# Kernel tuning notes

Measured on AMD Instinct MI355X. Metric: run time of the kernel, lower is better.

The kernel has to match this reference:

```python
import jax, jax.numpy as jnp
import numpy as np

BATCH = 4
N1 = 131072   # stage-1 voxels (total over batch)
N2 = 32768    # stage-2 (stride-2 downsampled) voxels
D_MODEL = 128
D_INNER = 2 * D_MODEL
D_STATE = 16
D_CONV = 4
DT_RANK = 8   # ceil(d_model / 16)
EPS = 1e-5


def _ln(x, g, b):
    mu = x.mean(-1, keepdims=True)
    v = ((x - mu) ** 2).mean(-1, keepdims=True)
    return (x - mu) * jax.lax.rsqrt(v + EPS) * g + b


def _causal_conv(x, w, b):
    # x: [B,L,Di], w: [Di,K] -> depthwise causal conv1d
    y = jax.lax.conv_general_dilated(
        x.transpose(0, 2, 1), w[:, None, :], (1,), [(D_CONV - 1, 0)],
        dimension_numbers=('NCH', 'OIH', 'NCH'), feature_group_count=D_INNER)
    return y.transpose(0, 2, 1) + b


def _mamba_block(x, ln_g, ln_b, in_w, conv_w, conv_b, xproj_w, dtproj_w, dtproj_b, A_log, Dp, out_w):
    # create_block: LayerNorm -> Mamba mixer (selective scan); returns hidden states
    h = _ln(x, ln_g, ln_b)
    xz = h @ in_w.T                          # [B,L,2*Di]
    xc, z = jnp.split(xz, 2, axis=-1)
    xc = jax.nn.silu(_causal_conv(xc, conv_w, conv_b))
    dbl = xc @ xproj_w.T                     # [B,L,dt_rank+2*d_state]
    dt = jax.nn.softplus(dbl[..., :DT_RANK] @ dtproj_w.T + dtproj_b)  # [B,L,Di]
    Bm = dbl[..., DT_RANK:DT_RANK + D_STATE]
    Cm = dbl[..., DT_RANK + D_STATE:]
    A = -jnp.exp(A_log)                      # [Di,ds]

    def step(hst, inp):
        dt_t, b_t, c_t, u_t = inp            # [B,Di],[B,ds],[B,ds],[B,Di]
        hst = jnp.exp(dt_t[..., None] * A) * hst + (dt_t * u_t)[..., None] * b_t[:, None, :]
        return hst, jnp.einsum('bds,bs->bd', hst, c_t)

    h0 = jnp.zeros((x.shape[0], D_INNER, D_STATE), x.dtype)
    xs = (dt.transpose(1, 0, 2), Bm.transpose(1, 0, 2), Cm.transpose(1, 0, 2), xc.transpose(1, 0, 2))
    _, ys = jax.lax.scan(step, h0, xs)       # ys: [L,B,Di]
    y = ys.transpose(1, 0, 2) + xc * Dp
    y = y * jax.nn.silu(z)
    return y @ out_w.T


def _mamba_params(key):
    ks = jax.random.split(key, 6)
    s = lambda k, sh, sc: jax.random.normal(k, sh, jnp.float32) * sc
    return dict(
        ln_g=jnp.ones((D_MODEL,), jnp.float32), ln_b=jnp.zeros((D_MODEL,), jnp.float32),
        in_w=s(ks[0], (2 * D_INNER, D_MODEL), 0.05),
        conv_w=s(ks[1], (D_INNER, D_CONV), 0.2), conv_b=jnp.zeros((D_INNER,), jnp.float32),
        xproj_w=s(ks[2], (DT_RANK + 2 * D_STATE, D_INNER), 0.05),
        dtproj_w=s(ks[3], (D_INNER, DT_RANK), 0.1), dtproj_b=s(ks[4], (D_INNER,), 0.1),
        A_log=jnp.log(jnp.tile(jnp.arange(1, D_STATE + 1, dtype=jnp.float32), (D_INNER, 1))),
        D=jnp.ones((D_INNER,), jnp.float32),
        out_w=s(ks[5], (D_MODEL, D_INNER), 0.05))


def setup_inputs():
    key = jax.random.key(0)
    k = jax.random.split(key, 10)
    inp = {
        'feats_s1': jax.random.normal(k[0], (N1, D_MODEL), jnp.float32),
        'feats_s2': jax.random.normal(k[1], (N2, D_MODEL), jnp.float32),
        'pos_s1': jax.random.uniform(k[2], (N1, 3), jnp.float32),
        'pos_s2': jax.random.uniform(k[3], (N2, 3), jnp.float32),
        'hilbert_s1': jax.random.randint(k[4], (N1,), 0, 1 << 30, jnp.int32),
        'hilbert_s2': jax.random.randint(k[5], (N2,), 0, 1 << 30, jnp.int32),
        'pe_w': jax.random.normal(k[6], (D_MODEL, 3), jnp.float32) * 0.1,
        'pe_b': jnp.zeros((D_MODEL,), jnp.float32),
        'norm_g': jnp.ones((D_MODEL,), jnp.float32), 'norm_b': jnp.zeros((D_MODEL,), jnp.float32),
        'normb_g': jnp.ones((D_MODEL,), jnp.float32), 'normb_b': jnp.zeros((D_MODEL,), jnp.float32),
    }
    for pref, kk in (('m1_', k[7]), ('m2_', k[8])):
        for n, v in _mamba_params(kk).items():
            inp[pref + n] = v
    return inp


def _forward(feats_s1, feats_s2, pos_s1, pos_s2, pe_w, pe_b, norm_g, norm_b, normb_g, normb_b,
             m1_ln_g, m1_ln_b, m1_in_w, m1_conv_w, m1_conv_b, m1_xproj_w, m1_dtproj_w, m1_dtproj_b, m1_A_log, m1_D, m1_out_w,
             m2_ln_g, m2_ln_b, m2_in_w, m2_conv_w, m2_conv_b, m2_xproj_w, m2_dtproj_w, m2_dtproj_b, m2_A_log, m2_D, m2_out_w,
             hilbert_s1, hilbert_s2):
    L1, L2 = N1 // BATCH, N2 // BATCH
    m1 = (m1_ln_g, m1_ln_b, m1_in_w, m1_conv_w, m1_conv_b, m1_xproj_w, m1_dtproj_w, m1_dtproj_b, m1_A_log, m1_D, m1_out_w)
    m2 = (m2_ln_g, m2_ln_b, m2_in_w, m2_conv_w, m2_conv_b, m2_xproj_w, m2_dtproj_w, m2_dtproj_b, m2_A_log, m2_D, m2_out_w)

    # stage 2: hilbert-order forward scan through mamba_layer1
    f2 = (feats_s2 + pos_s2 @ pe_w.T + pe_b).reshape(BATCH, L2, D_MODEL)
    o2 = jnp.argsort(hilbert_s2.reshape(BATCH, L2), axis=-1)          # inds_curt_to_next
    seq2 = jnp.take_along_axis(f2, o2[..., None], axis=1)
    out2 = _mamba_block(seq2, *m1)
    back2 = jnp.take_along_axis(out2, jnp.argsort(o2, axis=-1)[..., None], axis=1).reshape(N2, D_MODEL)
    out_s2 = _ln(back2, norm_g, norm_b)

    # stage 1: flipped hilbert-order (backward) scan through mamba_layer2
    f1 = (feats_s1 + pos_s1 @ pe_w.T + pe_b).reshape(BATCH, L1, D_MODEL)
    o1 = jnp.argsort(hilbert_s1.reshape(BATCH, L1), axis=-1)
    seq1 = jnp.take_along_axis(f1, o1[..., None], axis=1)[:, ::-1, :]
    out1 = _mamba_block(seq1, *m2)[:, ::-1, :]
    back1 = jnp.take_along_axis(out1, jnp.argsort(o1, axis=-1)[..., None], axis=1).reshape(N1, D_MODEL)
    out_s1 = _ln(back1, normb_g, normb_b)

    return jnp.concatenate([out_s1, out_s2], axis=0)   # [N1+N2, d_model]


def reference(feats_s1, feats_s2, pos_s1, pos_s2, pe_w, pe_b, norm_g, norm_b, normb_g, normb_b,
              m1_ln_g, m1_ln_b, m1_in_w, m1_conv_w, m1_conv_b, m1_xproj_w, m1_dtproj_w, m1_dtproj_b, m1_A_log, m1_D, m1_out_w,
              m2_ln_g, m2_ln_b, m2_in_w, m2_conv_w, m2_conv_b, m2_xproj_w, m2_dtproj_w, m2_dtproj_b, m2_A_log, m2_D, m2_out_w,
              hilbert_s1, hilbert_s2):
    return _forward(feats_s1, feats_s2, pos_s1, pos_s2, pe_w, pe_b, norm_g, norm_b, normb_g, normb_b,
                    m1_ln_g, m1_ln_b, m1_in_w, m1_conv_w, m1_conv_b, m1_xproj_w, m1_dtproj_w, m1_dtproj_b, m1_A_log, m1_D, m1_out_w,
                    m2_ln_g, m2_ln_b, m2_in_w, m2_conv_w, m2_conv_b, m2_xproj_w, m2_dtproj_w, m2_dtproj_b, m2_A_log, m2_D, m2_out_w,
                    hilbert_s1, hilbert_s2)
```

## Files before the change

kernel.cpp:

```cpp
#include <hip/hip_runtime.h>
#include <hip/hip_bf16.h>

#define DEV __device__ __forceinline__

constexpr int BATCH_ = 4;
constexpr int N1_ = 131072;
constexpr int N2_ = 32768;
constexpr int L1_ = N1_ / BATCH_;
constexpr int L2_ = N2_ / BATCH_;
constexpr int DM_ = 128;
constexpr int DI_ = 256;
constexpr int DS_ = 16;
constexpr int DTR_ = 8;
constexpr int TOT_ = N1_ + N2_;

constexpr int TA_ = 32;
constexpr int TAH_ = TA_ + 3;
constexpr int NTILE1_ = L1_ / TA_;
constexpr int NTILE2_ = L2_ / TA_;
constexpr int NTILES_ = 4 * NTILE1_ + 4 * NTILE2_;

constexpr int TS_ = 128;
constexpr int NCH1_ = L1_ / TS_;
constexpr int NCH2_ = L2_ / TS_;
constexpr int NCHUNKS_ = 4 * NCH1_ + 4 * NCH2_;

constexpr int NST_ = 160;

constexpr int PADR_ = 16;
constexpr int SR1_ = L1_ + 2 * PADR_;
constexpr int SR2_ = L2_ + 2 * PADR_;
constexpr int RTOT_ = 4 * SR1_ + 4 * SR2_;

constexpr int IN1_OFF = 0;
constexpr int IN2_OFF = 65536;
constexpr int XP1_OFF = 131072;
constexpr int XP2_OFF = 143360;
constexpr int OW1_OFF = 155648;
constexpr int OW2_OFF = 188416;
constexpr int W16_TOT = 221184;

typedef short short8 __attribute__((ext_vector_type(8)));
typedef float f32x4 __attribute__((ext_vector_type(4)));

struct MP {
  const float* ln_g; const float* ln_b; const float* in_w;
  const float* conv_w; const float* conv_b; const float* xproj_w;
  const float* dtproj_w; const float* dtproj_b; const float* A_log;
  const float* Dp; const float* out_w;
};

DEV float softplusf(float x) {
  return fmaxf(x, 0.f) + __logf(1.f + __expf(-fabsf(x)));
}

DEV unsigned short f2bf(float f) {
  unsigned u = __builtin_bit_cast(unsigned, f);
  u += 0x7fffu + ((u >> 16) & 1u);
  return (unsigned short)(u >> 16);
}
DEV float bf2f(unsigned short s) {
  unsigned u = ((unsigned)s) << 16;
  return __builtin_bit_cast(float, u);
}

DEV void sort_tile_info(int tile, int& seg, int& tis, int& slotbase) {
  if (tile < 128) { seg = tile >> 5; tis = tile & 31; slotbase = seg * L1_; }
  else { seg = 4 + ((tile - 128) >> 3); tis = (tile - 128) & 7; slotbase = N1_ + (seg - 4) * L2_; }
}

__global__ __launch_bounds__(256) void k_prep(
    const float* __restrict__ in_w1, const float* __restrict__ xp1,
    const float* __restrict__ ow1,
    const float* __restrict__ in_w2, const float* __restrict__ xp2,
    const float* __restrict__ ow2,
    unsigned short* __restrict__ w16)
{
  const int i = blockIdx.x * 256 + threadIdx.x;
  if (i >= W16_TOT) return;
  float v;
  if (i < IN2_OFF) v = in_w1[i - IN1_OFF];
  else if (i < XP1_OFF) v = in_w2[i - IN2_OFF];
  else if (i < XP2_OFF) {
    const int j = i - XP1_OFF; const int r = j >> 8;
    v = (r < 40) ? xp1[j] : 0.f;
  } else if (i < OW1_OFF) {
    const int j = i - XP2_OFF; const int r = j >> 8;
    v = (r < 40) ? xp2[j] : 0.f;
  } else if (i < OW2_OFF) v = ow1[i - OW1_OFF];
  else v = ow2[i - OW2_OFF];
  w16[i] = f2bf(v);
}

__global__ __launch_bounds__(256) void k_hist(
    const int* __restrict__ hil1, const int* __restrict__ hil2,
    const unsigned* __restrict__ ksrc, unsigned* __restrict__ histg,
    int shift, int pass0)
{
  const int tile = blockIdx.x;
  int seg, tis, slotbase;
  sort_tile_info(tile, seg, tis, slotbase);
  const int tid = threadIdx.x;
  __shared__ unsigned h[1024];
  #pragma unroll
  for (int i = 0; i < 4; ++i) h[i * 256 + tid] = 0;
  __syncthreads();
  #pragma unroll
  for (int it = 0; it < 4; ++it) {
    const int li = tis * 1024 + it * 256 + tid;
    unsigned k;
    if (pass0) k = (unsigned)(seg < 4 ? hil1[seg * L1_ + li] : hil2[(seg - 4) * L2_ + li]);
    else       k = ksrc[slotbase + li];
    atomicAdd(&h[(k >> shift) & 1023u], 1u);
  }
  __syncthreads();
  #pragma unroll
  for (int i = 0; i < 4; ++i)
    histg[tile * 1024 + i * 256 + tid] = h[i * 256 + tid];
}

__global__ __launch_bounds__(256) void k_scanoff(
    const unsigned* __restrict__ histg, unsigned* __restrict__ offg)
{
  const int seg = blockIdx.x;
  const int ntiles = seg < 4 ? 32 : 8;
  const int tilebase = seg < 4 ? seg * 32 : 128 + (seg - 4) * 8;
  const int tid = threadIdx.x;
  const int d0 = tid * 4;
  unsigned tot[4] = {0, 0, 0, 0};
  for (int t = 0; t < ntiles; ++t) {
    const unsigned* hp = &histg[(size_t)(tilebase + t) * 1024 + d0];
    tot[0] += hp[0]; tot[1] += hp[1]; tot[2] += hp[2]; tot[3] += hp[3];
  }
  unsigned lp[4]; unsigned s = 0;
  #pragma unroll
  for (int j = 0; j < 4; ++j) { lp[j] = s; s += tot[j]; }
  const int lane = tid & 63, wv = tid >> 6;
  unsigned inc = s;
  #pragma unroll
  for (int off = 1; off < 64; off <<= 1) {
    unsigned v = (unsigned)__shfl_up((int)inc, off, 64);
    if (lane >= off) inc += v;
  }
  __shared__ unsigned wsum[4];
  if (lane == 63) wsum[wv] = inc;
  __syncthreads();
  unsigned wbase = 0;
  for (int w = 0; w < 4; ++w) if (w < wv) wbase += wsum[w];
  const unsigned base = wbase + inc - s;
  #pragma unroll
  for (int j = 0; j < 4; ++j) {
    unsigned run = base + lp[j];
    for (int t = 0; t < ntiles; ++t) {
      offg[(size_t)(tilebase + t) * 1024 + d0 + j] = run;
      run += histg[(size_t)(tilebase + t) * 1024 + d0 + j];
    }
  }
}

__global__ __launch_bounds__(256) void k_scatter(
    const int* __restrict__ hil1, const int* __restrict__ hil2,
    const unsigned* __restrict__ ksrc, const int* __restrict__ isrc,
    const unsigned* __restrict__ offg,
    unsigned* __restrict__ kdst, int* __restrict__ idst,
    int* __restrict__ o_all, int shift, int pass0, int last)
{
  const int tile = blockIdx.x;
  int seg, tis, slotbase;
  sort_tile_info(tile, seg, tis, slotbase);
  const int tid = threadIdx.x;
  const int lane = tid & 63, wv = tid >> 6;
  __shared__ unsigned runb[1024];
  __shared__ unsigned wcnt[4 * 1024];
  #pragma unroll
  for (int i = 0; i < 4; ++i) runb[i * 256 + tid] = offg[(size_t)tile * 1024 + i * 256 + tid];
  #pragma unroll
  for (int it = 0; it < 4; ++it) {
    #pragma unroll
    for (int i = 0; i < 16; ++i) wcnt[i * 256 + tid] = 0;
    __syncthreads();
    const int li = tis * 1024 + it * 256 + tid;
    unsigned k; int v;
    if (pass0) {
      k = (unsigned)(seg < 4 ? hil1[seg * L1_ + li] : hil2[(seg - 4) * L2_ + li]);
      v = li;
    } else {
      k = ksrc[slotbase + li]; v = isrc[slotbase + li];
    }
    const unsigned d = (k >> shift) & 1023u;
    unsigned long long m = ~0ull;
    #pragma unroll
    for (int b = 0; b < 10; ++b) {
      const unsigned long long bb = __ballot((int)((d >> b) & 1u));
      m &= ((d >> b) & 1u) ? bb : ~bb;
    }
    const unsigned lrank = (unsigned)__popcll(m & ((1ull << lane) - 1ull));
    wcnt[wv * 1024 + d] = (unsigned)__popcll(m);
    __syncthreads();
    unsigned prior = runb[d];
    for (int w = 0; w < 3; ++w) if (w < wv) prior += wcnt[w * 1024 + d];
    const unsigned pos = prior + lrank;
    if (last) o_all[slotbase + pos] = v;
    else { kdst[slotbase + pos] = k; idst[slotbase + pos] = v; }
    __syncthreads();
    #pragma unroll
    for (int i = 0; i < 4; ++i) {
      const int dd = i * 256 + tid;
      runb[dd] += wcnt[dd] + wcnt[1024 + dd] + wcnt[2048 + dd] + wcnt[3072 + dd];
    }
    __syncthreads();
  }
}

__global__ __launch_bounds__(256) void k_gather(
    const float* __restrict__ feats1, const float* __restrict__ feats2,
    const float* __restrict__ pos1, const float* __restrict__ pos2,
    const float* __restrict__ pe_w, const float* __restrict__ pe_b,
    MP p1, MP p2, const int* __restrict__ o_all,
    unsigned* __restrict__ seq_g)
{
  const int wv = threadIdx.x >> 6, lane = threadIdx.x & 63;
  const int prow = blockIdx.x * 4 + wv;
  if (prow >= RTOT_) return;
  int seg, within;
  if (prow < 4 * SR1_) { seg = prow / SR1_; within = prow - seg * SR1_; }
  else { const int r = prow - 4 * SR1_; seg = 4 + r / SR2_; within = r - (seg - 4) * SR2_; }
  const bool is1 = seg < 4;
  const int b = is1 ? seg : seg - 4;
  const int L = is1 ? L1_ : L2_;
  const int p = within - PADR_;
  unsigned outw = 0;
  if (p >= 0 && p < L) {
    const int slotbase = is1 ? b * L1_ : N1_ + b * L2_;
    const int orig = o_all[slotbase + p];
    const MP P = is1 ? p2 : p1;
    const float* fr = (is1 ? feats1 + (size_t)b * L1_ * DM_
                           : feats2 + (size_t)b * L2_ * DM_) + (size_t)orig * DM_;
    const float* pr = (is1 ? pos1 + (size_t)b * L1_ * 3
                           : pos2 + (size_t)b * L2_ * 3) + (size_t)orig * 3;
    const int c0 = 2 * lane;
    const float2 f = *(const float2*)(fr + c0);
    const float q0 = pr[0], q1 = pr[1], q2 = pr[2];
    float x0 = f.x + q0 * pe_w[c0 * 3 + 0] + q1 * pe_w[c0 * 3 + 1] + q2 * pe_w[c0 * 3 + 2] + pe_b[c0];
    float x1 = f.y + q0 * pe_w[c0 * 3 + 3] + q1 * pe_w[c0 * 3 + 4] + q2 * pe_w[c0 * 3 + 5] + pe_b[c0 + 1];
    float s = x0 + x1, qq = x0 * x0 + x1 * x1;
    #pragma unroll
    for (int off = 32; off; off >>= 1) {
      s += __shfl_xor(s, off, 64);
      qq += __shfl_xor(qq, off, 64);
    }
    const float mu = s * (1.f / 128.f);
    const float rs = rsqrtf(qq * (1.f / 128.f) - mu * mu + 1e-5f);
    const unsigned short o0 = f2bf((x0 - mu) * rs * P.ln_g[c0]     + P.ln_b[c0]);
    const unsigned short o1 = f2bf((x1 - mu) * rs * P.ln_g[c0 + 1] + P.ln_b[c0 + 1]);
    outw = (unsigned)o0 | ((unsigned)o1 << 16);
  }
  seq_g[(size_t)prow * 64 + lane] = outw;
}

constexpr int HB_ = 136;
constexpr int XB_ = 264;
constexpr int OFF_HB16 = TAH_ * XB_ * 2;
constexpr int SMEM_A = OFF_HB16 + 48 * HB_ * 2;

__global__ __launch_bounds__(256) void k_phaseA(
    MP p1, MP p2,
    const unsigned short* __restrict__ seq_g,
    const unsigned short* __restrict__ w16,
    __hip_bfloat16* __restrict__ xc_g, __hip_bfloat16* __restrict__ z_g,
    float* __restrict__ dbl_g)
{
  const int blk = blockIdx.x;
  bool is1; int b, tile;
  if (blk < 4 * NTILE1_) { is1 = true; b = blk / NTILE1_; tile = blk % NTILE1_; }
  else { const int r = blk - 4 * NTILE1_; is1 = false; b = r / NTILE2_; tile = r % NTILE2_; }
  const int slotbase = is1 ? b * L1_ : N1_ + b * L2_;
  const MP P = is1 ? p2 : p1;
  const unsigned short* iw16 = w16 + (is1 ? IN2_OFF : IN1_OFF);
  const unsigned short* xp16 = w16 + (is1 ? XP2_OFF : XP1_OFF);
  const int segrow0 = is1 ? b * SR1_ : 4 * SR1_ + b * SR2_;
  const unsigned short* seq = seq_g + (size_t)segrow0 * DM_;
  const bool rev = is1;
  const int t0 = tile * TA_;
  const int pstart = rev ? t0 : t0 - 3;
  const int lsh = rev ? 0 : 3;

  __shared__ char smem[SMEM_A];
  unsigned short* xcb16 = (unsigned short*)smem;
  unsigned short* hb16 = (unsigned short*)(smem + OFF_HB16);
  unsigned short* xc16 = xcb16;

  const int tid = threadIdx.x;
  const int lane = tid & 63, wv = tid >> 6;
  const int l15 = lane & 15, quad = lane >> 4;

  {
    unsigned* hz = (unsigned*)hb16;
    for (int i = tid; i < 13 * (HB_ / 2); i += 256)
      hz[TAH_ * (HB_ / 2) + i] = 0;
    const unsigned short* src = seq + (size_t)(PADR_ + pstart) * DM_;
    #pragma unroll
    for (int i = tid; i < TAH_ * 16; i += 256) {
      const int r = i >> 4, c = (i & 15) * 8;
      *(uint4*)(hb16 + r * HB_ + c) = *(const uint4*)(src + (size_t)r * DM_ + c);
    }
  }
  __syncthreads();
  {
    short8 afr[3][4];
    #pragma unroll
    for (int mt = 0; mt < 3; ++mt)
      #pragma unroll
      for (int t = 0; t < 4; ++t)
        afr[mt][t] = *(const short8*)(hb16 + (mt * 16 + l15) * HB_ + t * 32 + quad * 8);
    for (int nn = 0; nn < 8; ++nn) {
      const int ntile = nn * 4 + wv;
      f32x4 acc[3];
      #pragma unroll
      for (int mt = 0; mt < 3; ++mt) acc[mt] = (f32x4){0.f, 0.f, 0.f, 0.f};
      #pragma unroll
      for (int t = 0; t < 4; ++t) {
        const short8 bfr = *(const short8*)(iw16 + (size_t)(ntile * 16 + l15) * DM_ + t * 32 + quad * 8);
        #pragma unroll
        for (int mt = 0; mt < 3; ++mt)
          acc[mt] = __builtin_amdgcn_mfma_f32_16x16x32_bf16(afr[mt][t], bfr, acc[mt], 0, 0, 0);
      }
      const int col = ntile * 16 + l15;
      if (col < 256) {
        #pragma unroll
        for (int mt = 0; mt < 3; ++mt)
          #pragma unroll
          for (int r = 0; r < 4; ++r) {
            const int row = mt * 16 + quad * 4 + r;
            if (row < TAH_) xcb16[row * XB_ + col] = f2bf(acc[mt][r]);
          }
      } else {
        #pragma unroll
        for (int mt = 0; mt < 3; ++mt)
          #pragma unroll
          for (int r = 0; r < 4; ++r) {
            const int row = mt * 16 + quad * 4 + r;
            const int m = row - lsh;
            if (m >= 0 && m < TA_)
              z_g[(size_t)(slotbase + t0 + m) * DI_ + (col - 256)] = __float2bfloat16(acc[mt][r]);
          }
      }
    }
  }
  __syncthreads();
  {
    const int d = tid;
    const float w0 = P.conv_w[d * 4 + 0], w1 = P.conv_w[d * 4 + 1],
                w2 = P.conv_w[d * 4 + 2], w3 = P.conv_w[d * 4 + 3];
    const float cb = P.conv_b[d];
    float x0 = bf2f(xcb16[0 * XB_ + d]), x1 = bf2f(xcb16[1 * XB_ + d]),
          x2 = bf2f(xcb16[2 * XB_ + d]);
    #pragma unroll
    for (int m = 0; m < TA_; ++m) {
      const float x3 = bf2f(xcb16[(m + 3) * XB_ + d]);
      float v;
      if (rev) v = w3 * x0 + w2 * x1 + w1 * x2 + w0 * x3;
      else     v = w0 * x0 + w1 * x1 + w2 * x2 + w3 * x3;
      v += cb;
      v = v * (1.f / (1.f + __expf(-v)));
      const unsigned short vb = f2bf(v);
      xc_g[(size_t)(slotbase + t0 + m) * DI_ + d] = __builtin_bit_cast(__hip_bfloat16, vb);
      xcb16[m * XB_ + d] = vb;
      x0 = x1; x1 = x2; x2 = x3;
    }
  }
  __syncthreads();
  if (wv < 3) {
    f32x4 acc0 = (f32x4){0.f,0.f,0.f,0.f}, acc1 = acc0;
    #pragma unroll
    for (int t = 0; t < 8; ++t) {
      const short8 bfr = *(const short8*)(xp16 + (size_t)(wv * 16 + l15) * DI_ + t * 32 + quad * 8);
      const short8 a0 = *(const short8*)(xc16 + (l15) * XB_ + t * 32 + quad * 8);
      const short8 a1 = *(const short8*)(xc16 + (16 + l15) * XB_ + t * 32 + quad * 8);
      acc0 = __builtin_amdgcn_mfma_f32_16x16x32_bf16(a0, bfr, acc0, 0, 0, 0);
      acc1 = __builtin_amdgcn_mfma_f32_16x16x32_bf16(a1, bfr, acc1, 0, 0, 0);
    }
    const int col = wv * 16 + l15;
    if (col < 40) {
      #pragma unroll
      for (int r = 0; r < 4; ++r) {
        dbl_g[(size_t)(slotbase + t0 + quad * 4 + r) * 40 + col] = acc0[r];
        dbl_g[(size_t)(slotbase + t0 + 16 + quad * 4 + r) * 40 + col] = acc1[r];
      }
    }
  }
}

struct ScanP {
  float Av[DS_]; float A0; bool fast;
  float dtw[DTR_]; float dtb;
};
DEV void load_scanp(const MP& P, int d, ScanP& sp) {
  #pragma unroll
  for (int s = 0; s < DS_; ++s) sp.Av[s] = -__expf(P.A_log[d * DS_ + s]);
  sp.A0 = sp.Av[0];
  bool f = true;
  #pragma unroll
  for (int s = 0; s < DS_; ++s)
    f = f && (fabsf(sp.Av[s] - (float)(s + 1) * sp.A0) <= 1e-3f * (float)(s + 1));
  sp.fast = f;
  #pragma unroll
  for (int r = 0; r < DTR_; ++r) sp.dtw[r] = P.dtproj_w[d * DTR_ + r];
  sp.dtb = P.dtproj_b[d];
}
DEV float dt_from(const float4& q0, const float4& q1, const ScanP& sp) {
  const float dtraw = sp.dtb
      + q0.x*sp.dtw[0] + q0.y*sp.dtw[1] + q0.z*sp.dtw[2] + q0.w*sp.dtw[3]
      + q1.x*sp.dtw[4] + q1.y*sp.dtw[5] + q1.z*sp.dtw[6] + q1.w*sp.dtw[7];
  return softplusf(dtraw);
}

__global__ __launch_bounds__(256) void k_scan1(
    MP p1, MP p2,
    const __hip_bfloat16* __restrict__ xc_g, const float* __restrict__ dbl_g,
    float* __restrict__ hloc, float* __restrict__ sumdt_g)
{
  const int blk = blockIdx.x;
  bool is1; int b, pc;
  if (blk < 4 * NCH1_) { is1 = true; b = blk / NCH1_; pc = blk % NCH1_; }
  else { const int r = blk - 4 * NCH1_; is1 = false; b = r / NCH2_; pc = r % NCH2_; }
  const MP P = is1 ? p2 : p1;
  const int L = is1 ? L1_ : L2_;
  const bool rev = is1;
  const int slotbase = is1 ? b * L1_ : N1_ + b * L2_;
  const int d = threadIdx.x;
  ScanP sp; load_scanp(P, d, sp);
  const unsigned short* xcp = (const unsigned short*)xc_g;
  float h[DS_];
  #pragma unroll
  for (int s = 0; s < DS_; ++s) h[s] = 0.f;
  float sdt = 0.f;
  const int s0 = rev ? (L - (pc + 1) * TS_) : pc * TS_;
  const int dp = rev ? -1 : 1;
  int slot = slotbase + (rev ? (s0 + TS_ - 1) : s0);
  if (sp.fast) {
    const float* dr = dbl_g + (size_t)slot * 40;
    float4 q0 = *(const float4*)dr, q1 = *(const float4*)(dr + 4);
    float4 Bv[4];
    #pragma unroll
    for (int j = 0; j < 4; ++j) Bv[j] = *(const float4*)(dr + 8 + 4 * j);
    float u = bf2f(xcp[(size_t)slot * DI_ + d]);
    for (int i = 0; i < TS_; ++i) {
      const int nslot = (i + 1 < TS_) ? slot + dp : slot;
      const float* nr = dbl_g + (size_t)nslot * 40;
      float4 nq0 = *(const float4*)nr, nq1 = *(const float4*)(nr + 4);
      float4 nB[4];
      #pragma unroll
      for (int j = 0; j < 4; ++j) nB[j] = *(const float4*)(nr + 8 + 4 * j);
      const float nu = bf2f(xcp[(size_t)nslot * DI_ + d]);
      const float dt = dt_from(q0, q1, sp);
      const float du = dt * u;
      sdt += dt;
      const float e1 = __expf(dt * sp.A0);
      const float e2 = e1 * e1, e3 = e2 * e1, e4 = e2 * e2;
      float base = 1.f;
      #pragma unroll
      for (int j = 0; j < 4; ++j) {
        const float m1 = base * e1, m2 = base * e2, m3 = base * e3, m4 = base * e4;
        h[4*j+0] = m1 * h[4*j+0] + du * Bv[j].x;
        h[4*j+1] = m2 * h[4*j+1] + du * Bv[j].y;
        h[4*j+2] = m3 * h[4*j+2] + du * Bv[j].z;
        h[4*j+3] = m4 * h[4*j+3] + du * Bv[j].w;
        base = m4;
      }
      slot = nslot; q0 = nq0; q1 = nq1; u = nu;
      #pragma unroll
      for (int j = 0; j < 4; ++j) Bv[j] = nB[j];
    }
  } else {
    for (int i = 0; i < TS_; ++i) {
      const float* dr = dbl_g + (size_t)slot * 40;
      const float4 q0 = *(const float4*)dr, q1 = *(const float4*)(dr + 4);
      const float dt = dt_from(q0, q1, sp);
      const float u = bf2f(xcp[(size_t)slot * DI_ + d]);
      const float du = dt * u;
      sdt += dt;
      float Bvv[16];
      #pragma unroll
      for (int j = 0; j < 4; ++j) *(float4*)&Bvv[4*j] = *(const float4*)(dr + 8 + 4*j);
      #pragma unroll
      for (int s = 0; s < DS_; ++s)
        h[s] = __expf(dt * sp.Av[s]) * h[s] + du * Bvv[s];
      slot += dp;
    }
  }
  float* hl = hloc + (size_t)blk * DS_ * DI_;
  #pragma unroll
  for (int s = 0; s < DS_; ++s) hl[s * DI_ + d] = h[s];
  sumdt_g[(size_t)blk * DI_ + d] = sdt;
}

__global__ __launch_bounds__(256) void k_scan2(
    MP p1, MP p2, const float* __restrict__ hloc,
    const float* __restrict__ sumdt_g, float* __restrict__ hin)
{
  const int seq = blockIdx.x >> 4;
  const int s = blockIdx.x & 15;
  const bool is1 = seq < 4;
  const int b = is1 ? seq : seq - 4;
  const MP P = is1 ? p2 : p1;
  const int nch = is1 ? NCH1_ : NCH2_;
  const int chbase = is1 ? b * NCH1_ : 4 * NCH1_ + b * NCH2_;
  const int d = threadIdx.x;
  const float A = -__expf(P.A_log[d * DS_ + s]);
  float carry = 0.f;
  for (int pc = 0; pc < nch; ++pc) {
    const size_t idx = (size_t)(chbase + pc);
    const float sdt = sumdt_g[idx * DI_ + d];
    hin[idx * DS_ * DI_ + s * DI_ + d] = carry;
    carry = __expf(A * sdt) * carry + hloc[idx * DS_ * DI_ + s * DI_ + d];
  }
}

__global__ __launch_bounds__(256) void k_scan3(
    MP p1, MP p2,
    const __hip_bfloat16* __restrict__ xc_g, const float* __restrict__ dbl_g,
    const float* __restrict__ hin, __hip_bfloat16* zv_g)
{
  const int blk = blockIdx.x;
  bool is1; int b, pc;
  if (blk < 4 * NCH1_) { is1 = true; b = blk / NCH1_; pc = blk % NCH1_; }
  else { const int r = blk - 4 * NCH1_; is1 = false; b = r / NCH2_; pc = r % NCH2_; }
  const MP P = is1 ? p2 : p1;
  const int L = is1 ? L1_ : L2_;
  const bool rev = is1;
  const int slotbase = is1 ? b * L1_ : N1_ + b * L2_;
  const int d = threadIdx.x;
  ScanP sp; load_scanp(P, d, sp);
  const float Dp = P.Dp[d];
  const unsigned short* xcp = (const unsigned short*)xc_g;
  unsigned short* zvp = (unsigned short*)zv_g;
  float h[DS_];
  const float* hi = hin + (size_t)blk * DS_ * DI_;
  #pragma unroll
  for (int s = 0; s < DS_; ++s) h[s] = hi[s * DI_ + d];
  const int s0 = rev ? (L - (pc + 1) * TS_) : pc * TS_;
  const int dp = rev ? -1 : 1;
  int slot = slotbase + (rev ? (s0 + TS_ - 1) : s0);
  if (sp.fast) {
    const float* dr = dbl_g + (size_t)slot * 40;
    float4 q0 = *(const float4*)dr, q1 = *(const float4*)(dr + 4);
    float4 Bv[4], Cv[4];
    #pragma unroll
    for (int j = 0; j < 4; ++j) {
      Bv[j] = *(const float4*)(dr + 8 + 4 * j);
      Cv[j] = *(const float4*)(dr + 24 + 4 * j);
    }
    float u = bf2f(xcp[(size_t)slot * DI_ + d]);
    float zv = bf2f(zvp[(size_t)slot * DI_ + d]);
    for (int i = 0; i < TS_; ++i) {
      const int nslot = (i + 1 < TS_) ? slot + dp : slot;
      const float* nr = dbl_g + (size_t)nslot * 40;
      float4 nq0 = *(const float4*)nr, nq1 = *(const float4*)(nr + 4);
      float4 nB[4], nC[4];
      #pragma unroll
      for (int j = 0; j < 4; ++j) {
        nB[j] = *(const float4*)(nr + 8 + 4 * j);
        nC[j] = *(const float4*)(nr + 24 + 4 * j);
      }
      const float nu = bf2f(xcp[(size_t)nslot * DI_ + d]);
      const float nz = bf2f(zvp[(size_t)nslot * DI_ + d]);
      const float dt = dt_from(q0, q1, sp);
      const float du = dt * u;
      const float e1 = __expf(dt * sp.A0);
      const float e2 = e1 * e1, e3 = e2 * e1, e4 = e2 * e2;
      float base = 1.f;
      float y = 0.f;
      #pragma unroll
      for (int j = 0; j < 4; ++j) {
        const float m1 = base * e1, m2 = base * e2, m3 = base * e3, m4 = base * e4;
        h[4*j+0] = m1 * h[4*j+0] + du * Bv[j].x;  y += h[4*j+0] * Cv[j].x;
        h[4*j+1] = m2 * h[4*j+1] + du * Bv[j].y;  y += h[4*j+1] * Cv[j].y;
        h[4*j+2] = m3 * h[4*j+2] + du * Bv[j].z;  y += h[4*j+2] * Cv[j].z;
        h[4*j+3] = m4 * h[4*j+3] + du * Bv[j].w;  y += h[4*j+3] * Cv[j].w;
        base = m4;
      }
      const float sg = zv / (1.f + __expf(-zv));
      zvp[(size_t)slot * DI_ + d] = f2bf((y + u * Dp) * sg);
      slot = nslot; q0 = nq0; q1 = nq1; u = nu; zv = nz;
      #pragma unroll
      for (int j = 0; j < 4; ++j) { Bv[j] = nB[j]; Cv[j] = nC[j]; }
    }
  } else {
    for (int i = 0; i < TS_; ++i) {
      const float* dr = dbl_g + (size_t)slot * 40;
      const float4 q0 = *(const float4*)dr, q1 = *(const float4*)(dr + 4);
      const float dt = dt_from(q0, q1, sp);
      const float u = bf2f(xcp[(size_t)slot * DI_ + d]);
      const float zv = bf2f(zvp[(size_t)slot * DI_ + d]);
      const float du = dt * u;
      float Bvv[16], Cvv[16];
      #pragma unroll
      for (int j = 0; j < 4; ++j) {
        *(float4*)&Bvv[4*j] = *(const float4*)(dr + 8 + 4*j);
        *(float4*)&Cvv[4*j] = *(const float4*)(dr + 24 + 4*j);
      }
      float y = 0.f;
      #pragma unroll
      for (int s = 0; s < DS_; ++s) {
        h[s] = __expf(dt * sp.Av[s]) * h[s] + du * Bvv[s];
        y += h[s] * Cvv[s];
      }
      const float sg = zv / (1.f + __expf(-zv));
      zvp[(size_t)slot * DI_ + d] = f2bf((y + u * Dp) * sg);
      slot += dp;
    }
  }
}

constexpr int OB_ = 132;
__global__ __launch_bounds__(256) void k_final(
    const __hip_bfloat16* __restrict__ v_g, const int* __restrict__ o_all,
    const unsigned short* __restrict__ w16,
    const float* __restrict__ norm_g, const float* __restrict__ norm_b,
    const float* __restrict__ normb_g, const float* __restrict__ normb_b,
    float* __restrict__ out)
{
  const int blk = blockIdx.x;
  bool is1; int b, tile;
  if (blk < 4 * NTILE1_) { is1 = true; b = blk / NTILE1_; tile = blk % NTILE1_; }
  else { const int r = blk - 4 * NTILE1_; is1 = false; b = r / NTILE2_; tile = r % NTILE2_; }
  const unsigned short* W = w16 + (is1 ? OW2_OFF : OW1_OFF);
  const float* gg = is1 ? normb_g : norm_g;
  const float* gb = is1 ? normb_b : norm_b;
  const int slotbase = is1 ? b * L1_ : N1_ + b * L2_;
  const int t0 = tile * TA_;
  __shared__ float obuf[TA_ * OB_];
  const int tid = threadIdx.x;
  const int lane = tid & 63, wv = tid >> 6;
  const int l15 = lane & 15, quad = lane >> 4;
  {
    const unsigned short* vp = (const unsigned short*)v_g + (size_t)(slotbase + t0) * DI_;
    f32x4 acc00 = (f32x4){0.f,0.f,0.f,0.f}, acc01 = acc00, acc10 = acc00, acc11 = acc00;
    #pragma unroll
    for (int t = 0; t < 8; ++t) {
      const short8 a0 = *(const short8*)(vp + (size_t)(l15) * DI_ + t * 32 + quad * 8);
      const short8 a1 = *(const short8*)(vp + (size_t)(16 + l15) * DI_ + t * 32 + quad * 8);
      const short8 b0 = *(const short8*)(W + (size_t)((wv) * 16 + l15) * DI_ + t * 32 + quad * 8);
      const short8 b1 = *(const short8*)(W + (size_t)((wv + 4) * 16 + l15) * DI_ + t * 32 + quad * 8);
      acc00 = __builtin_amdgcn_mfma_f32_16x16x32_bf16(a0, b0, acc00, 0, 0, 0);
      acc01 = __builtin_amdgcn_mfma_f32_16x16x32_bf16(a1, b0, acc01, 0, 0, 0);
      acc10 = __builtin_amdgcn_mfma_f32_16x16x32_bf16(a0, b1, acc10, 0, 0, 0);
      acc11 = __builtin_amdgcn_mfma_f32_16x16x32_bf16(a1, b1, acc11, 0, 0, 0);
    }
    const int col0 = wv * 16 + l15;
    const int col1 = (wv + 4) * 16 + l15;
    #pragma unroll
    for (int r = 0; r < 4; ++r) {
      obuf[(quad * 4 + r) * OB_ + col0] = acc00[r];
      obuf[(16 + quad * 4 + r) * OB_ + col0] = acc01[r];
      obuf[(quad * 4 + r) * OB_ + col1] = acc10[r];
      obuf[(16 + quad * 4 + r) * OB_ + col1] = acc11[r];
    }
  }
  __syncthreads();
  {
    for (int m = wv; m < TA_; m += 4) {
      float x0 = obuf[m * OB_ + lane], x1 = obuf[m * OB_ + lane + 64];
      float s = x0 + x1, q = x0 * x0 + x1 * x1;
      #pragma unroll
      for (int off = 32; off; off >>= 1) {
        s += __shfl_xor(s, off, 64);
        q += __shfl_xor(q, off, 64);
      }
      const float mu = s * (1.f / 128.f);
      const float rs = rsqrtf(q * (1.f / 128.f) - mu * mu + 1e-5f);
      const int orig = o_all[slotbase + t0 + m];
      float* orow = out + (size_t)(slotbase + orig) * DM_;
      orow[lane]      = (x0 - mu) * rs * gg[lane]      + gb[lane];
      orow[lane + 64] = (x1 - mu) * rs * gg[lane + 64] + gb[lane + 64];
    }
  }
}

extern "C" void kernel_launch(void* const* d_in, const int* in_sizes, int n_in,
                              void* d_out, int out_size, void* d_ws, size_t ws_size,
                              hipStream_t stream)
{
  (void)in_sizes; (void)n_in; (void)out_size; (void)ws_size;
  const float* feats1 = (const float*)d_in[0];
  const float* feats2 = (const float*)d_in[1];
  const float* pos1   = (const float*)d_in[2];
  const float* pos2   = (const float*)d_in[3];
  const int*   hil1   = (const int*)d_in[4];
  const int*   hil2   = (const int*)d_in[5];
  const float* pe_w   = (const float*)d_in[6];
  const float* pe_b   = (const float*)d_in[7];
  const float* norm_g  = (const float*)d_in[8];
  const float* norm_b  = (const float*)d_in[9];
  const float* normb_g = (const float*)d_in[10];
  const float* normb_b = (const float*)d_in[11];
  MP p1 { (const float*)d_in[12], (const float*)d_in[13], (const float*)d_in[14],
          (const float*)d_in[15], (const float*)d_in[16], (const float*)d_in[17],
          (const float*)d_in[18], (const float*)d_in[19], (const float*)d_in[20],
          (const float*)d_in[21], (const float*)d_in[22] };
  MP p2 { (const float*)d_in[23], (const float*)d_in[24], (const float*)d_in[25],
          (const float*)d_in[26], (const float*)d_in[27], (const float*)d_in[28],
          (const float*)d_in[29], (const float*)d_in[30], (const float*)d_in[31],
          (const float*)d_in[32], (const float*)d_in[33] };

  char* w = (char*)d_ws;
  auto take = [&](size_t bytes) -> char* {
    char* p = w; w += (bytes + 255) & ~(size_t)255; return p;
  };
  int* o_all = (int*)take((size_t)TOT_ * 4);
  unsigned* kA = (unsigned*)take((size_t)TOT_ * 4);
  int* iA = (int*)take((size_t)TOT_ * 4);
  unsigned* kB = (unsigned*)take((size_t)TOT_ * 4);
  int* iB = (int*)take((size_t)TOT_ * 4);
  unsigned* histg = (unsigned*)take((size_t)NST_ * 1024 * 4);
  unsigned* offg  = (unsigned*)take((size_t)NST_ * 1024 * 4);
  __hip_bfloat16* xc = (__hip_bfloat16*)take((size_t)TOT_ * DI_ * 2);
  __hip_bfloat16* vzb = (__hip_bfloat16*)take((size_t)TOT_ * DI_ * 2);
  float* dbl = (float*)take((size_t)TOT_ * 40 * 4);
  float* hloc = (float*)take((size_t)NCHUNKS_ * DS_ * DI_ * 4);
  float* hin  = (float*)take((size_t)NCHUNKS_ * DS_ * DI_ * 4);
  float* sdt  = (float*)take((size_t)NCHUNKS_ * DI_ * 4);
  unsigned short* w16 = (unsigned short*)take((size_t)W16_TOT * 2);
  unsigned* seq = (unsigned*)take((size_t)RTOT_ * DM_ * 2);

  hipLaunchKernelGGL(k_prep, dim3((W16_TOT + 255) / 256), dim3(256), 0, stream,
                     p1.in_w, p1.xproj_w, p1.out_w, p2.in_w, p2.xproj_w, p2.out_w, w16);
  hipLaunchKernelGGL(k_hist, dim3(NST_), dim3(256), 0, stream,
                     hil1, hil2, kB, histg, 0, 1);
  hipLaunchKernelGGL(k_scanoff, dim3(8), dim3(256), 0, stream, histg, offg);
  hipLaunchKernelGGL(k_scatter, dim3(NST_), dim3(256), 0, stream,
                     hil1, hil2, kB, iB, offg, kB, iB, o_all, 0, 1, 0);
  hipLaunchKernelGGL(k_hist, dim3(NST_), dim3(256), 0, stream,
                     hil1, hil2, kB, histg, 10, 0);
  hipLaunchKernelGGL(k_scanoff, dim3(8), dim3(256), 0, stream, histg, offg);
  hipLaunchKernelGGL(k_scatter, dim3(NST_), dim3(256), 0, stream,
                     hil1, hil2, kB, iB, offg, kA, iA, o_all, 10, 0, 0);
  hipLaunchKernelGGL(k_hist, dim3(NST_), dim3(256), 0, stream,
                     hil1, hil2, kA, histg, 20, 0);
  hipLaunchKernelGGL(k_scanoff, dim3(8), dim3(256), 0, stream, histg, offg);
  hipLaunchKernelGGL(k_scatter, dim3(NST_), dim3(256), 0, stream,
                     hil1, hil2, kA, iA, offg, kB, iB, o_all, 20, 0, 1);

  hipLaunchKernelGGL(k_gather, dim3((RTOT_ + 3) / 4), dim3(256), 0, stream,
                     feats1, feats2, pos1, pos2, pe_w, pe_b, p1, p2, o_all, seq);
  hipLaunchKernelGGL(k_phaseA, dim3(NTILES_), dim3(256), 0, stream,
                     p1, p2, (const unsigned short*)seq, w16, xc, vzb, dbl);
  hipLaunchKernelGGL(k_scan1, dim3(NCHUNKS_), dim3(256), 0, stream,
                     p1, p2, xc, dbl, hloc, sdt);
  hipLaunchKernelGGL(k_scan2, dim3(128), dim3(256), 0, stream,
                     p1, p2, hloc, sdt, hin);
  hipLaunchKernelGGL(k_scan3, dim3(NCHUNKS_), dim3(256), 0, stream,
                     p1, p2, xc, dbl, hin, vzb);
  hipLaunchKernelGGL(k_final, dim3(NTILES_), dim3(256), 0, stream,
                     vzb, o_all, w16, norm_g, norm_b, normb_g, normb_b,
                     (float*)d_out);
}
```

Baseline: 881.1 us.

## Halve scan chunk size, precompute silu(z), drop manual prefetch, reuse workspace

Scan chunks shrink from 128 to 64 steps, so the chunked scan launches twice as many blocks and each serial chain is shorter, at the cost of a longer sequential carry pass in k_scan2. The silu gate on z is now computed in the phase-A epilogue and no longer in the scan3 inner loop. The hand-written software prefetch in scan1 and scan3 is replaced by plain loads with unroll 2, which lowers register pressure. k_scan2 writes carries in place into hloc so the separate hin buffer is gone, and the sort scratch buffers alias the gathered-sequence buffer to shrink the workspace footprint.

After: 913.8 us. +3.7%, slower.

```diff
diff --git a/kernel.cpp b/kernel.cpp
--- a/kernel.cpp
+++ b/kernel.cpp
@@ -20,7 +20,7 @@
 constexpr int NTILE2_ = L2_ / TA_;
 constexpr int NTILES_ = 4 * NTILE1_ + 4 * NTILE2_;
 
-constexpr int TS_ = 128;
+constexpr int TS_ = 64;
 constexpr int NCH1_ = L1_ / TS_;
 constexpr int NCH2_ = L2_ / TS_;
 constexpr int NCHUNKS_ = 4 * NCH1_ + 4 * NCH2_;
@@ -341,8 +341,11 @@
           for (int r = 0; r < 4; ++r) {
             const int row = mt * 16 + quad * 4 + r;
             const int m = row - lsh;
-            if (m >= 0 && m < TA_)
-              z_g[(size_t)(slotbase + t0 + m) * DI_ + (col - 256)] = __float2bfloat16(acc[mt][r]);
+            if (m >= 0 && m < TA_) {
+              const float zz = acc[mt][r];
+              const float sg = zz / (1.f + __expf(-zz));
+              z_g[(size_t)(slotbase + t0 + m) * DI_ + (col - 256)] = __float2bfloat16(sg);
+            }
           }
       }
     }
@@ -439,20 +442,14 @@
   const int dp = rev ? -1 : 1;
   int slot = slotbase + (rev ? (s0 + TS_ - 1) : s0);
   if (sp.fast) {
-    const float* dr = dbl_g + (size_t)slot * 40;
-    float4 q0 = *(const float4*)dr, q1 = *(const float4*)(dr + 4);
-    float4 Bv[4];
-    #pragma unroll
-    for (int j = 0; j < 4; ++j) Bv[j] = *(const float4*)(dr + 8 + 4 * j);
-    float u = bf2f(xcp[(size_t)slot * DI_ + d]);
+    #pragma unroll 2
     for (int i = 0; i < TS_; ++i) {
-      const int nslot = (i + 1 < TS_) ? slot + dp : slot;
-      const float* nr = dbl_g + (size_t)nslot * 40;
-      float4 nq0 = *(const float4*)nr, nq1 = *(const float4*)(nr + 4);
-      float4 nB[4];
-      #pragma unroll
-      for (int j = 0; j < 4; ++j) nB[j] = *(const float4*)(nr + 8 + 4 * j);
-      const float nu = bf2f(xcp[(size_t)nslot * DI_ + d]);
+      const float* dr = dbl_g + (size_t)slot * 40;
+      const float4 q0 = *(const float4*)dr, q1 = *(const float4*)(dr + 4);
+      const float u = bf2f(xcp[(size_t)slot * DI_ + d]);
+      float4 Bv[4];
+      #pragma unroll
+      for (int j = 0; j < 4; ++j) Bv[j] = *(const float4*)(dr + 8 + 4 * j);
       const float dt = dt_from(q0, q1, sp);
       const float du = dt * u;
       sdt += dt;
@@ -468,9 +465,7 @@
         h[4*j+3] = m4 * h[4*j+3] + du * Bv[j].w;
         base = m4;
       }
-      slot = nslot; q0 = nq0; q1 = nq1; u = nu;
-      #pragma unroll
-      for (int j = 0; j < 4; ++j) Bv[j] = nB[j];
+      slot += dp;
     }
   } else {
     for (int i = 0; i < TS_; ++i) {
@@ -496,8 +491,8 @@
 }
 
 __global__ __launch_bounds__(256) void k_scan2(
-    MP p1, MP p2, const float* __restrict__ hloc,
-    const float* __restrict__ sumdt_g, float* __restrict__ hin)
+    MP p1, MP p2, float* __restrict__ hloc,
+    const float* __restrict__ sumdt_g)
 {
   const int seq = blockIdx.x >> 4;
   const int s = blockIdx.x & 15;
@@ -512,8 +507,9 @@
   for (int pc = 0; pc < nch; ++pc) {
     const size_t idx = (size_t)(chbase + pc);
     const float sdt = sumdt_g[idx * DI_ + d];
-    hin[idx * DS_ * DI_ + s * DI_ + d] = carry;
-    carry = __expf(A * sdt) * carry + hloc[idx * DS_ * DI_ + s * DI_ + d];
+    const float hl = hloc[idx * DS_ * DI_ + s * DI_ + d];
+    hloc[idx * DS_ * DI_ + s * DI_ + d] = carry;
+    carry = __expf(A * sdt) * carry + hl;
   }
 }
 
@@ -543,34 +539,25 @@
   const int dp = rev ? -1 : 1;
   int slot = slotbase + (rev ? (s0 + TS_ - 1) : s0);
   if (sp.fast) {
-    const float* dr = dbl_g + (size_t)slot * 40;
-    float4 q0 = *(const float4*)dr, q1 = *(const float4*)(dr + 4);
-    float4 Bv[4], Cv[4];
-    #pragma unroll
-    for (int j = 0; j < 4; ++j) {
-      Bv[j] = *(const float4*)(dr + 8 + 4 * j);
-      Cv[j] = *(const float4*)(dr + 24 + 4 * j);
-    }
-    float u = bf2f(xcp[(size_t)slot * DI_ + d]);
-    float zv = bf2f(zvp[(size_t)slot * DI_ + d]);
+    float sz = bf2f(zvp[(size_t)slot * DI_ + d]);
+    #pragma unroll 2
     for (int i = 0; i < TS_; ++i) {
       const int nslot = (i + 1 < TS_) ? slot + dp : slot;
-      const float* nr = dbl_g + (size_t)nslot * 40;
-      float4 nq0 = *(const float4*)nr, nq1 = *(const float4*)(nr + 4);
-      float4 nB[4], nC[4];
+      const float nsz = bf2f(zvp[(size_t)nslot * DI_ + d]);
+      const float* dr = dbl_g + (size_t)slot * 40;
+      const float4 q0 = *(const float4*)dr, q1 = *(const float4*)(dr + 4);
+      const float u = bf2f(xcp[(size_t)slot * DI_ + d]);
+      float4 Bv[4], Cv[4];
       #pragma unroll
       for (int j = 0; j < 4; ++j) {
-        nB[j] = *(const float4*)(nr + 8 + 4 * j);
-        nC[j] = *(const float4*)(nr + 24 + 4 * j);
-      }
-      const float nu = bf2f(xcp[(size_t)nslot * DI_ + d]);
-      const float nz = bf2f(zvp[(size_t)nslot * DI_ + d]);
+        Bv[j] = *(const float4*)(dr + 8 + 4 * j);
+        Cv[j] = *(const float4*)(dr + 24 + 4 * j);
+      }
       const float dt = dt_from(q0, q1, sp);
       const float du = dt * u;
       const float e1 = __expf(dt * sp.A0);
       const float e2 = e1 * e1, e3 = e2 * e1, e4 = e2 * e2;
-      float base = 1.f;
-      float y = 0.f;
+      float base = 1.f, y = 0.f;
       #pragma unroll
       for (int j = 0; j < 4; ++j) {
         const float m1 = base * e1, m2 = base * e2, m3 = base * e3, m4 = base * e4;
@@ -580,11 +567,8 @@
         h[4*j+3] = m4 * h[4*j+3] + du * Bv[j].w;  y += h[4*j+3] * Cv[j].w;
         base = m4;
       }
-      const float sg = zv / (1.f + __expf(-zv));
-      zvp[(size_t)slot * DI_ + d] = f2bf((y + u * Dp) * sg);
-      slot = nslot; q0 = nq0; q1 = nq1; u = nu; zv = nz;
-      #pragma unroll
-      for (int j = 0; j < 4; ++j) { Bv[j] = nB[j]; Cv[j] = nC[j]; }
+      zvp[(size_t)slot * DI_ + d] = f2bf((y + u * Dp) * sz);
+      slot = nslot; sz = nsz;
     }
   } else {
     for (int i = 0; i < TS_; ++i) {
@@ -592,7 +576,7 @@
       const float4 q0 = *(const float4*)dr, q1 = *(const float4*)(dr + 4);
       const float dt = dt_from(q0, q1, sp);
       const float u = bf2f(xcp[(size_t)slot * DI_ + d]);
-      const float zv = bf2f(zvp[(size_t)slot * DI_ + d]);
+      const float sz = bf2f(zvp[(size_t)slot * DI_ + d]);
       const float du = dt * u;
       float Bvv[16], Cvv[16];
       #pragma unroll
@@ -606,8 +590,7 @@
         h[s] = __expf(dt * sp.Av[s]) * h[s] + du * Bvv[s];
         y += h[s] * Cvv[s];
       }
-      const float sg = zv / (1.f + __expf(-zv));
-      zvp[(size_t)slot * DI_ + d] = f2bf((y + u * Dp) * sg);
+      zvp[(size_t)slot * DI_ + d] = f2bf((y + u * Dp) * sz);
       slot += dp;
     }
   }
@@ -709,20 +692,20 @@
     char* p = w; w += (bytes + 255) & ~(size_t)255; return p;
   };
   int* o_all = (int*)take((size_t)TOT_ * 4);
-  unsigned* kA = (unsigned*)take((size_t)TOT_ * 4);
-  int* iA = (int*)take((size_t)TOT_ * 4);
-  unsigned* kB = (unsigned*)take((size_t)TOT_ * 4);
-  int* iB = (int*)take((size_t)TOT_ * 4);
-  unsigned* histg = (unsigned*)take((size_t)NST_ * 1024 * 4);
-  unsigned* offg  = (unsigned*)take((size_t)NST_ * 1024 * 4);
+  char* uni = take((size_t)RTOT_ * DM_ * 2);
+  unsigned* kA = (unsigned*)(uni);
+  int*      iA = (int*)     (uni + (size_t)TOT_ * 4);
+  unsigned* kB = (unsigned*)(uni + (size_t)TOT_ * 8);
+  int*      iB = (int*)     (uni + (size_t)TOT_ * 12);
+  unsigned* histg = (unsigned*)(uni + (size_t)TOT_ * 16);
+  unsigned* offg  = (unsigned*)(uni + (size_t)TOT_ * 16 + (size_t)NST_ * 1024 * 4);
+  unsigned* seq = (unsigned*)uni;
   __hip_bfloat16* xc = (__hip_bfloat16*)take((size_t)TOT_ * DI_ * 2);
   __hip_bfloat16* vzb = (__hip_bfloat16*)take((size_t)TOT_ * DI_ * 2);
   float* dbl = (float*)take((size_t)TOT_ * 40 * 4);
   float* hloc = (float*)take((size_t)NCHUNKS_ * DS_ * DI_ * 4);
-  float* hin  = (float*)take((size_t)NCHUNKS_ * DS_ * DI_ * 4);
   float* sdt  = (float*)take((size_t)NCHUNKS_ * DI_ * 4);
   unsigned short* w16 = (unsigned short*)take((size_t)W16_TOT * 2);
-  unsigned* seq = (unsigned*)take((size_t)RTOT_ * DM_ * 2);
 
   hipLaunchKernelGGL(k_prep, dim3((W16_TOT + 255) / 256), dim3(256), 0, stream,
                      p1.in_w, p1.xproj_w, p1.out_w, p2.in_w, p2.xproj_w, p2.out_w, w16);
@@ -749,9 +732,9 @@
   hipLaunchKernelGGL(k_scan1, dim3(NCHUNKS_), dim3(256), 0, stream,
                      p1, p2, xc, dbl, hloc, sdt);
   hipLaunchKernelGGL(k_scan2, dim3(128), dim3(256), 0, stream,
-                     p1, p2, hloc, sdt, hin);
+                     p1, p2, hloc, sdt);
   hipLaunchKernelGGL(k_scan3, dim3(NCHUNKS_), dim3(256), 0, stream,
-                     p1, p2, xc, dbl, hin, vzb);
+                     p1, p2, xc, dbl, hloc, vzb);
   hipLaunchKernelGGL(k_final, dim3(NTILES_), dim3(256), 0, stream,
                      vzb, o_all, w16, norm_g, norm_b, normb_g, normb_b,
                      (float*)d_out);
```
